# Performance work log

Measured on AMD Instinct MI355X. Metric: run time of the kernel, lower is better.

## Reference

```python
import jax, jax.numpy as jnp
import numpy as np

NX = 1024
NF = 4096
B = 8
S = 4096

def setup_inputs() -> dict:
    key = jax.random.key(0)
    k1, k2, k3, k4 = jax.random.split(key, 4)
    x = jax.random.normal(k1, (B, S, NX), dtype=jnp.float32)
    # symmetric int8 weights in [-127, 127]
    qw = jax.random.randint(k2, (NX, NF), -127, 128, dtype=jnp.int32).astype(jnp.int8)
    weight_scale = jax.random.uniform(k3, (), dtype=jnp.float32) * 0.01 + 1e-4
    bias = jax.random.normal(k4, (NF,), dtype=jnp.float32)
    return {"x": x, "quantized_weight": qw, "weight_scale": weight_scale, "bias": bias}

def reference(x, quantized_weight, weight_scale, bias):
    # dequantize: (int8 -> fp32) * scale, zero_point = 0
    w = quantized_weight.astype(jnp.float32) * weight_scale  # [nx, nf]
    size_out = x.shape[:-1] + (w.shape[-1],)
    out = x.reshape(-1, x.shape[-1]) @ w + bias               # addmm
    return out.reshape(size_out)
```

## Files before the change

kernel.cpp:

```cpp
#include <hip/hip_runtime.h>
#include <hip/hip_bf16.h>
#include <stdint.h>
#include <stddef.h>

typedef __bf16 bf16_t;
typedef __attribute__((ext_vector_type(8))) __bf16 bf16x8;
typedef __attribute__((ext_vector_type(4))) __bf16 bf16x4;
typedef __attribute__((ext_vector_type(4))) float f32x4;
typedef __attribute__((ext_vector_type(4))) int i32x4;
typedef __attribute__((ext_vector_type(16))) char c8x16;

#define M_DIM 32768
#define N_DIM 4096
#define K_DIM 1024
#define NT 8

static __device__ __forceinline__ void gload16(const void* g, void* s) {
  __builtin_amdgcn_global_load_lds(
      (const __attribute__((address_space(1))) void*)g,
      (__attribute__((address_space(3))) void*)s,
      16, 0, 0);
}

__global__ void quant_x_kernel(const float* __restrict__ x,
                               int8_t* __restrict__ xq,
                               float* __restrict__ xs) {
  const int row = blockIdx.x * 4 + (threadIdx.x >> 6);
  const int lane = threadIdx.x & 63;
  const float* src = x + (long)row * K_DIM + lane * 16;
  float4 v[4];
#pragma unroll
  for (int i = 0; i < 4; ++i) v[i] = ((const float4*)src)[i];
  float am = 0.f;
#pragma unroll
  for (int i = 0; i < 4; ++i) {
    am = fmaxf(am, fmaxf(fmaxf(fabsf(v[i].x), fabsf(v[i].y)),
                         fmaxf(fabsf(v[i].z), fabsf(v[i].w))));
  }
#pragma unroll
  for (int off = 32; off; off >>= 1) am = fmaxf(am, __shfl_xor(am, off));
  const float sq = am > 0.f ? 127.f / am : 0.f;
  c8x16 q;
#pragma unroll
  for (int i = 0; i < 4; ++i) {
    const float* f = (const float*)&v[i];
#pragma unroll
    for (int j = 0; j < 4; ++j) {
      int qi = (int)rintf(f[j] * sq);
      qi = qi > 127 ? 127 : (qi < -127 ? -127 : qi);
      q[i * 4 + j] = (char)qi;
    }
  }
  *(c8x16*)(xq + (long)row * K_DIM + lane * 16) = q;
  if (lane == 0) xs[row] = am * (1.f / 127.f);
}

__global__ void cvt_w_i8_kernel(const int* __restrict__ qw,
                                int8_t* __restrict__ wq) {
  __shared__ char t[64][80];
  const int bk = blockIdx.x & 15;
  const int bn = blockIdx.x >> 4;
  const int k0 = bk * 64, n0 = bn * 64;
  const int tid = threadIdx.x;
  {
    const int kl = tid >> 2;
    const int nc = (tid & 3) * 16;
    const int* src = qw + (long)(k0 + kl) * N_DIM + n0 + nc;
#pragma unroll
    for (int c = 0; c < 4; ++c) {
      i32x4 v = *(const i32x4*)(src + c * 4);
#pragma unroll
      for (int j = 0; j < 4; ++j) t[nc + c * 4 + j][kl] = (char)v[j];
    }
  }
  __syncthreads();
  {
    const int nl = tid >> 2;
    const int kc = (tid & 3) * 16;
    *(i32x4*)(wq + (long)(n0 + nl) * K_DIM + k0 + kc) =
        *(const i32x4*)&t[nl][kc];
  }
}

__global__ __launch_bounds__(256, 2) void gemm_i8_kernel(
    const int8_t* __restrict__ Aq, const int8_t* __restrict__ Bq,
    const float* __restrict__ xs, const float* __restrict__ scale_p,
    const float* __restrict__ bias, float* __restrict__ C) {
  __shared__ __align__(16) char lds[65536];

  const int xcd = blockIdx.x & 7;
  const int slot = blockIdx.x >> 3;
  const int tn = (xcd << 2) | (slot & 3);
  const int tm = slot >> 2;

  const int tid = threadIdx.x;
  const int wave = tid >> 6;
  const int lane = tid & 63;
  const int lr = lane & 15;
  const int lg = lane >> 4;
  const int wm = wave >> 1;
  const int wn = wave & 1;

  const long aRow0 = (long)tm * 128;
  const long bRow0 = (long)tn * 128;

  const int s = tid >> 3;
  const int scol = ((tid & 7) ^ (s & 7)) * 16;
  const int8_t* aS = Aq + (aRow0 + s) * K_DIM + scol;
  const int8_t* bS = Bq + (bRow0 + s) * K_DIM + scol;
  char* sBase = lds + wave * 1024;

#define STG_A(b, h, t)                                                      \
  do {                                                                      \
    gload16(aS + (long)((h) * 32) * K_DIM + (t) * 128,                      \
            sBase + (b) * 32768 + (h) * 8192);                              \
    gload16(aS + (long)((h) * 32 + 64) * K_DIM + (t) * 128,                 \
            sBase + (b) * 32768 + (h) * 8192 + 4096);                       \
  } while (0)
#define STG_B(b, h, t)                                                      \
  do {                                                                      \
    gload16(bS + (long)((h) * 32) * K_DIM + (t) * 128,                      \
            sBase + (b) * 32768 + 16384 + (h) * 8192);                      \
    gload16(bS + (long)((h) * 32 + 64) * K_DIM + (t) * 128,                 \
            sBase + (b) * 32768 + 16384 + (h) * 8192 + 4096);               \
  } while (0)

  const int ck0 = ((0 + lg) ^ (lr & 7)) << 4;
  const int ck1 = ((4 + lg) ^ (lr & 7)) << 4;

#define LDA(m, kk)                                                           \
  (*(const i32x4*)(lds + bb + ((m) >> 1) * 8192 +                            \
                   (wm * 32 + ((m) & 1) * 16 + lr) * 128 +                   \
                   ((kk) ? ck1 : ck0)))
#define LDB(n, kk)                                                           \
  (*(const i32x4*)(lds + bb + 16384 + ((n) >> 1) * 8192 +                    \
                   (wn * 32 + ((n) & 1) * 16 + lr) * 128 +                   \
                   ((kk) ? ck1 : ck0)))

#define SYNC(Nimm)                                           \
  do {                                                       \
    asm volatile("s_waitcnt vmcnt(" #Nimm ")" ::: "memory"); \
    __builtin_amdgcn_s_barrier();                            \
    __builtin_amdgcn_sched_barrier(0);                       \
  } while (0)

  i32x4 acc[4][4] = {};
  i32x4 bfr[4][2], afr[2][2];

#define MFMA_Q(mbase, nbase)                                                  \
  do {                                                                        \
    __builtin_amdgcn_s_setprio(1);                                            \
    _Pragma("unroll") for (int mm = 0; mm < 2; ++mm)                          \
    _Pragma("unroll") for (int nn = 0; nn < 2; ++nn)                          \
    _Pragma("unroll") for (int kk = 0; kk < 2; ++kk)                          \
      acc[(mbase) + mm][(nbase) + nn] =                                       \
          __builtin_amdgcn_mfma_i32_16x16x64_i8(                              \
              afr[mm][kk], bfr[(nbase) + nn][kk],                             \
              acc[(mbase) + mm][(nbase) + nn], 0, 0, 0);                      \
    __builtin_amdgcn_s_setprio(0);                                            \
  } while (0)

#define RD_B01()                                                              \
  _Pragma("unroll") for (int n = 0; n < 2; ++n) {                             \
    bfr[n][0] = LDB(n, 0);                                                    \
    bfr[n][1] = LDB(n, 1);                                                    \
  }
#define RD_B23()                                                              \
  _Pragma("unroll") for (int n = 2; n < 4; ++n) {                             \
    bfr[n][0] = LDB(n, 0);                                                    \
    bfr[n][1] = LDB(n, 1);                                                    \
  }
#define RD_A01()                                                              \
  _Pragma("unroll") for (int mm = 0; mm < 2; ++mm) {                          \
    afr[mm][0] = LDA(mm, 0);                                                  \
    afr[mm][1] = LDA(mm, 1);                                                  \
  }
#define RD_A23()                                                              \
  _Pragma("unroll") for (int mm = 0; mm < 2; ++mm) {                          \
    afr[mm][0] = LDA(mm + 2, 0);                                              \
    afr[mm][1] = LDA(mm + 2, 1);                                              \
  }

  STG_A(0, 0, 0);
  STG_B(0, 0, 0);
  STG_B(0, 1, 0);
  STG_A(0, 1, 0);

#pragma unroll 1
  for (int t = 0; t < NT - 1; ++t) {
    const int b = t & 1;
    const int nb = b ^ 1;
    const int bb = b * 32768;
    SYNC(4);
    RD_B01();
    RD_A01();
    STG_A(nb, 0, t + 1);
    MFMA_Q(0, 0);
    SYNC(4);
    RD_B23();
    STG_B(nb, 0, t + 1);
    MFMA_Q(0, 2);
    SYNC(4);
    RD_A23();
    STG_B(nb, 1, t + 1);
    MFMA_Q(2, 0);
    STG_A(nb, 1, t + 1);
    MFMA_Q(2, 2);
  }
  {
    const int bb = 32768;
    SYNC(4);
    RD_B01();
    RD_A01();
    MFMA_Q(0, 0);
    SYNC(2);
    RD_B23();
    MFMA_Q(0, 2);
    SYNC(0);
    RD_A23();
    MFMA_Q(2, 0);
    MFMA_Q(2, 2);
  }

#undef STG_A
#undef STG_B
#undef LDA
#undef LDB
#undef SYNC
#undef MFMA_Q
#undef RD_B01
#undef RD_B23
#undef RD_A01
#undef RD_A23

  const float ws = *scale_p;
  const int col_base = (tn << 7) + wn * 64;
  const int row_base = (tm << 7) + wm * 64 + lg * 4;
  float4 svw[4];
#pragma unroll
  for (int m = 0; m < 4; ++m) {
    float4 sv = *(const float4*)(xs + row_base + m * 16);
    svw[m].x = sv.x * ws; svw[m].y = sv.y * ws;
    svw[m].z = sv.z * ws; svw[m].w = sv.w * ws;
  }
#pragma unroll
  for (int n = 0; n < 4; ++n) {
    const int col = col_base + n * 16 + lr;
    const float bv = bias[col];
#pragma unroll
    for (int m = 0; m < 4; ++m) {
      float* cp = C + (long)(row_base + m * 16) * N_DIM + col;
      const float* sw = (const float*)&svw[m];
#pragma unroll
      for (int j = 0; j < 4; ++j)
        __builtin_nontemporal_store((float)acc[m][n][j] * sw[j] + bv,
                                    cp + (long)j * N_DIM);
    }
  }
}

__global__ void cvt_w_kernel(const int* __restrict__ qw, bf16_t* __restrict__ wt) {
  __shared__ bf16_t t[64][72];
  const int bk = blockIdx.x & 15;
  const int bn = blockIdx.x >> 4;
  const int k0 = bk * 64, n0 = bn * 64;
  const int tid = threadIdx.x;
  {
    const int kl = tid >> 2;
    const int nc = (tid & 3) * 16;
    const int* src = qw + (long)(k0 + kl) * N_DIM + n0 + nc;
#pragma unroll
    for (int c = 0; c < 4; ++c) {
      i32x4 v = *(const i32x4*)(src + c * 4);
#pragma unroll
      for (int j = 0; j < 4; ++j)
        t[nc + c * 4 + j][kl] = (bf16_t)(float)v[j];
    }
  }
  __syncthreads();
  {
    const int nl = tid >> 2;
    const int kc = (tid & 3) * 16;
    bf16_t* dst = wt + (long)(n0 + nl) * K_DIM + k0 + kc;
#pragma unroll
    for (int j = 0; j < 16; ++j) dst[j] = t[nl][kc + j];
  }
}

__global__ __launch_bounds__(256, 2) void gemm_fb_kernel(
    const float* __restrict__ Af, const bf16_t* __restrict__ Bt,
    const float* __restrict__ scale_p, const float* __restrict__ bias,
    float* __restrict__ C) {
  __shared__ bf16_t lA[128][64];
  __shared__ bf16_t lB[128][64];
  const int nwg = gridDim.x;
  int wg = blockIdx.x;
  wg = (wg & 7) * (nwg >> 3) + (wg >> 3);
  const int tm = wg & 255;
  const int tn = wg >> 8;
  const int tid = threadIdx.x;
  const int wave = tid >> 6;
  const int lane = tid & 63;
  const int lr = lane & 15;
  const int lg = lane >> 4;
  const int wm = wave >> 1;
  const int wn = wave & 1;
  const long aRow0 = (long)tm * 128;
  const long bRow0 = (long)tn * 128;
  const bf16_t* bSrc = Bt + (bRow0 + (tid >> 3)) * K_DIM + (tid & 7) * 8;
  char* ldsB = (char*)&lB[0][0] + wave * 1024;
  f32x4 acc[4][4] = {};
  for (int k0 = 0; k0 < K_DIM; k0 += 64) {
    __syncthreads();
#pragma unroll
    for (int j = 0; j < 8; ++j) {
      const int e = j * 1024 + tid * 4;
      const int row = e >> 6;
      const int col = e & 63;
      float4 v = *(const float4*)(Af + (aRow0 + row) * K_DIM + k0 + col);
      bf16x4 o;
      o[0] = (__bf16)v.x; o[1] = (__bf16)v.y; o[2] = (__bf16)v.z; o[3] = (__bf16)v.w;
      *(bf16x4*)((char*)&lA[0][0] + (size_t)e * 2) = o;
    }
#pragma unroll
    for (int i = 0; i < 4; ++i)
      gload16(bSrc + (long)i * 32 * K_DIM + k0, ldsB + i * 4096);
    __syncthreads();
#pragma unroll
    for (int kk = 0; kk < 2; ++kk) {
      bf16x8 af[4], bg[4];
#pragma unroll
      for (int m = 0; m < 4; ++m)
        af[m] = *(const bf16x8*)&lA[wm * 64 + m * 16 + lr][kk * 32 + lg * 8];
#pragma unroll
      for (int n = 0; n < 4; ++n)
        bg[n] = *(const bf16x8*)&lB[wn * 64 + n * 16 + lr][kk * 32 + lg * 8];
#pragma unroll
      for (int m = 0; m < 4; ++m)
#pragma unroll
        for (int n = 0; n < 4; ++n)
          acc[m][n] = __builtin_amdgcn_mfma_f32_16x16x32_bf16(af[m], bg[n], acc[m][n], 0, 0, 0);
    }
  }
  const float s = *scale_p;
  const int col0 = (tn << 7) + wn * 64;
  const int row0 = (tm << 7) + wm * 64 + lg * 4;
#pragma unroll
  for (int n = 0; n < 4; ++n) {
    const int col = col0 + n * 16 + lr;
    const float bv = bias[col];
#pragma unroll
    for (int m = 0; m < 4; ++m) {
      float* cp = C + (long)(row0 + m * 16) * N_DIM + col;
#pragma unroll
      for (int j = 0; j < 4; ++j)
        cp[(long)j * N_DIM] = acc[m][n][j] * s + bv;
    }
  }
}

extern "C" void kernel_launch(void* const* d_in, const int* in_sizes, int n_in,
                              void* d_out, int out_size, void* d_ws, size_t ws_size,
                              hipStream_t stream) {
  const float* x = (const float*)d_in[0];
  const int* qw = (const int*)d_in[1];
  const float* scale = (const float*)d_in[2];
  const float* bias = (const float*)d_in[3];
  float* out = (float*)d_out;

  const size_t wq_bytes = (size_t)N_DIM * K_DIM;
  const size_t xs_off = wq_bytes;
  const size_t xq_off = wq_bytes + (256u << 10);
  const size_t need = xq_off + (size_t)M_DIM * K_DIM;

  if (ws_size >= need) {
    int8_t* wq = (int8_t*)d_ws;
    float* xs = (float*)((char*)d_ws + xs_off);
    int8_t* xq = (int8_t*)((char*)d_ws + xq_off);
    cvt_w_i8_kernel<<<dim3((K_DIM / 64) * (N_DIM / 64)), dim3(256), 0, stream>>>(qw, wq);
    quant_x_kernel<<<dim3(M_DIM / 4), dim3(256), 0, stream>>>(x, xq, xs);
    gemm_i8_kernel<<<dim3((M_DIM / 128) * (N_DIM / 128)), dim3(256), 0, stream>>>(
        xq, wq, xs, scale, bias, out);
  } else {
    bf16_t* wt = (bf16_t*)d_ws;
    cvt_w_kernel<<<dim3((K_DIM / 64) * (N_DIM / 64)), dim3(256), 0, stream>>>(qw, wt);
    gemm_fb_kernel<<<dim3((M_DIM / 128) * (N_DIM / 128)), dim3(256), 0, stream>>>(
        x, wt, scale, bias, out);
  }
}
```

Measured before the change: 209.0 us.

## Load B fragments directly from global memory, halving LDS and raising occupancy

B tiles no longer go through LDS. Each wave reads its B fragments straight from global memory into registers every K step, and only A is double-buffered in LDS. This halves the shared memory per block to 32 KB and raises the launch bound to 3 blocks per CU for more occupancy, and it also cuts the number of barriers per iteration. The trade-off is that B is re-read by both wave-rows from global or L2 with no prefetch ahead of use, so global load latency is exposed right before the MFMAs, and register pressure rises under the tighter launch bound.

```diff
diff --git a/kernel.cpp b/kernel.cpp
--- a/kernel.cpp
+++ b/kernel.cpp
@@ -82,11 +82,11 @@
   }
 }
 
-__global__ __launch_bounds__(256, 2) void gemm_i8_kernel(
+__global__ __launch_bounds__(256, 3) void gemm_i8_kernel(
     const int8_t* __restrict__ Aq, const int8_t* __restrict__ Bq,
     const float* __restrict__ xs, const float* __restrict__ scale_p,
     const float* __restrict__ bias, float* __restrict__ C) {
-  __shared__ __align__(16) char lds[65536];
+  __shared__ __align__(16) char lds[32768];
 
   const int xcd = blockIdx.x & 7;
   const int slot = blockIdx.x >> 3;
@@ -107,22 +107,14 @@
   const int s = tid >> 3;
   const int scol = ((tid & 7) ^ (s & 7)) * 16;
   const int8_t* aS = Aq + (aRow0 + s) * K_DIM + scol;
-  const int8_t* bS = Bq + (bRow0 + s) * K_DIM + scol;
   char* sBase = lds + wave * 1024;
 
 #define STG_A(b, h, t)                                                      \
   do {                                                                      \
     gload16(aS + (long)((h) * 32) * K_DIM + (t) * 128,                      \
-            sBase + (b) * 32768 + (h) * 8192);                              \
+            sBase + (b) * 16384 + (h) * 8192);                              \
     gload16(aS + (long)((h) * 32 + 64) * K_DIM + (t) * 128,                 \
-            sBase + (b) * 32768 + (h) * 8192 + 4096);                       \
-  } while (0)
-#define STG_B(b, h, t)                                                      \
-  do {                                                                      \
-    gload16(bS + (long)((h) * 32) * K_DIM + (t) * 128,                      \
-            sBase + (b) * 32768 + 16384 + (h) * 8192);                      \
-    gload16(bS + (long)((h) * 32 + 64) * K_DIM + (t) * 128,                 \
-            sBase + (b) * 32768 + 16384 + (h) * 8192 + 4096);               \
+            sBase + (b) * 16384 + (h) * 8192 + 4096);                       \
   } while (0)
 
   const int ck0 = ((0 + lg) ^ (lr & 7)) << 4;
@@ -132,10 +124,10 @@
   (*(const i32x4*)(lds + bb + ((m) >> 1) * 8192 +                            \
                    (wm * 32 + ((m) & 1) * 16 + lr) * 128 +                   \
                    ((kk) ? ck1 : ck0)))
-#define LDB(n, kk)                                                           \
-  (*(const i32x4*)(lds + bb + 16384 + ((n) >> 1) * 8192 +                    \
-                   (wn * 32 + ((n) & 1) * 16 + lr) * 128 +                   \
-                   ((kk) ? ck1 : ck0)))
+
+  const int8_t* bP = Bq + (bRow0 + wn * 64 + lr) * (long)K_DIM + lg * 16;
+#define LDB_G(n, kk, t) \
+  (*(const i32x4*)(bP + (long)(n) * 16 * K_DIM + (t) * 128 + (kk) * 64))
 
 #define SYNC(Nimm)                                           \
   do {                                                       \
@@ -147,28 +139,21 @@
   i32x4 acc[4][4] = {};
   i32x4 bfr[4][2], afr[2][2];
 
-#define MFMA_Q(mbase, nbase)                                                  \
+#define MFMA_ROWS(mbase)                                                      \
   do {                                                                        \
     __builtin_amdgcn_s_setprio(1);                                            \
     _Pragma("unroll") for (int mm = 0; mm < 2; ++mm)                          \
-    _Pragma("unroll") for (int nn = 0; nn < 2; ++nn)                          \
+    _Pragma("unroll") for (int nn = 0; nn < 4; ++nn)                          \
     _Pragma("unroll") for (int kk = 0; kk < 2; ++kk)                          \
-      acc[(mbase) + mm][(nbase) + nn] =                                       \
-          __builtin_amdgcn_mfma_i32_16x16x64_i8(                              \
-              afr[mm][kk], bfr[(nbase) + nn][kk],                             \
-              acc[(mbase) + mm][(nbase) + nn], 0, 0, 0);                      \
+      acc[(mbase) + mm][nn] = __builtin_amdgcn_mfma_i32_16x16x64_i8(          \
+          afr[mm][kk], bfr[nn][kk], acc[(mbase) + mm][nn], 0, 0, 0);          \
     __builtin_amdgcn_s_setprio(0);                                            \
   } while (0)
 
-#define RD_B01()                                                              \
-  _Pragma("unroll") for (int n = 0; n < 2; ++n) {                             \
-    bfr[n][0] = LDB(n, 0);                                                    \
-    bfr[n][1] = LDB(n, 1);                                                    \
-  }
-#define RD_B23()                                                              \
-  _Pragma("unroll") for (int n = 2; n < 4; ++n) {                             \
-    bfr[n][0] = LDB(n, 0);                                                    \
-    bfr[n][1] = LDB(n, 1);                                                    \
+#define RD_B(t)                                                               \
+  _Pragma("unroll") for (int n = 0; n < 4; ++n) {                             \
+    bfr[n][0] = LDB_G(n, 0, t);                                               \
+    bfr[n][1] = LDB_G(n, 1, t);                                               \
   }
 #define RD_A01()                                                              \
   _Pragma("unroll") for (int mm = 0; mm < 2; ++mm) {                          \
@@ -182,54 +167,40 @@
   }
 
   STG_A(0, 0, 0);
-  STG_B(0, 0, 0);
-  STG_B(0, 1, 0);
   STG_A(0, 1, 0);
 
 #pragma unroll 1
   for (int t = 0; t < NT - 1; ++t) {
     const int b = t & 1;
     const int nb = b ^ 1;
-    const int bb = b * 32768;
-    SYNC(4);
-    RD_B01();
+    const int bb = b * 16384;
+    SYNC(2);
+    RD_B(t);
+    STG_A(nb, 0, t + 1);
     RD_A01();
-    STG_A(nb, 0, t + 1);
-    MFMA_Q(0, 0);
-    SYNC(4);
-    RD_B23();
-    STG_B(nb, 0, t + 1);
-    MFMA_Q(0, 2);
-    SYNC(4);
+    MFMA_ROWS(0);
+    SYNC(2);
+    STG_A(nb, 1, t + 1);
     RD_A23();
-    STG_B(nb, 1, t + 1);
-    MFMA_Q(2, 0);
-    STG_A(nb, 1, t + 1);
-    MFMA_Q(2, 2);
-  }
-  {
-    const int bb = 32768;
-    SYNC(4);
-    RD_B01();
+    MFMA_ROWS(2);
+  }
+  {
+    const int bb = 16384;
+    SYNC(2);
+    RD_B(NT - 1);
     RD_A01();
-    MFMA_Q(0, 0);
-    SYNC(2);
-    RD_B23();
-    MFMA_Q(0, 2);
+    MFMA_ROWS(0);
     SYNC(0);
     RD_A23();
-    MFMA_Q(2, 0);
-    MFMA_Q(2, 2);
+    MFMA_ROWS(2);
   }
 
 #undef STG_A
-#undef STG_B
 #undef LDA
-#undef LDB
+#undef LDB_G
 #undef SYNC
-#undef MFMA_Q
-#undef RD_B01
-#undef RD_B23
+#undef MFMA_ROWS
+#undef RD_B
 #undef RD_A01
 #undef RD_A23
 
```

Result: slower. 324.1 us (+55.1%).
